# Performance work log

Measured on AMD Instinct MI355X. Metric: run time of the kernel, lower is better.

The kernel has to match this reference:

```python
import jax, jax.numpy as jnp
import numpy as np

SAMPLE_RATE = 16000
LOW_CUTOFF = 3400.0   # max(cutoff_freq) -> lowpass stage
HIGH_CUTOFF = 300.0   # min(cutoff_freq) -> highpass stage
Q = 0.7071067811865476  # torchaudio default Q = 1/sqrt(2)


def _lowpass_coeffs(cutoff, sr):
    w0 = 2.0 * np.pi * cutoff / sr
    alpha = np.sin(w0) / (2.0 * Q)
    cw = np.cos(w0)
    b0 = (1.0 - cw) / 2.0
    b1 = 1.0 - cw
    b2 = b0
    a0 = 1.0 + alpha
    a1 = -2.0 * cw
    a2 = 1.0 - alpha
    return tuple(np.float32(c / a0) for c in (b0, b1, b2, a1, a2))


def _highpass_coeffs(cutoff, sr):
    w0 = 2.0 * np.pi * cutoff / sr
    alpha = np.sin(w0) / (2.0 * Q)
    cw = np.cos(w0)
    b0 = (1.0 + cw) / 2.0
    b1 = -(1.0 + cw)
    b2 = b0
    a0 = 1.0 + alpha
    a1 = -2.0 * cw
    a2 = 1.0 - alpha
    return tuple(np.float32(c / a0) for c in (b0, b1, b2, a1, a2))


def _biquad(x, coeffs):
    """Direct-form-II-transposed biquad along the last (time) axis.
    x: [B, C, T]. Matches torchaudio lfilter with a0-normalized coeffs,
    followed by the torchaudio default clamp to [-1, 1]."""
    b0, b1, b2, a1, a2 = (jnp.asarray(c, x.dtype) for c in coeffs)
    xt = jnp.moveaxis(x, -1, 0)  # [T, B, C] for time scan

    def step(carry, xi):
        s1, s2 = carry
        y = b0 * xi + s1
        s1n = b1 * xi - a1 * y + s2
        s2n = b2 * xi - a2 * y
        return (s1n, s2n), y

    zeros = jnp.zeros(x.shape[:-1], x.dtype)
    _, yt = jax.lax.scan(step, (zeros, zeros), xt)
    y = jnp.moveaxis(yt, 0, -1)  # back to [B, C, T]
    return jnp.clip(y, -1.0, 1.0)


def setup_inputs() -> dict:
    key = jax.random.key(0)
    # scale down so the post-filter clamp to [-1,1] rarely saturates (audio-like amplitudes)
    waveform = 0.1 * jax.random.normal(key, (32, 2, 480000), dtype=jnp.float32)
    return {"waveform": waveform}


def reference(waveform):
    # bandpass = lowpass(max cutoff) then highpass(min cutoff)
    y = _biquad(waveform, _lowpass_coeffs(LOW_CUTOFF, SAMPLE_RATE))
    y = _biquad(y, _highpass_coeffs(HIGH_CUTOFF, SAMPLE_RATE))
    return y
```

## Files before the change

kernel.cpp:

```cpp
#include <hip/hip_runtime.h>
#include <math.h>


#define LCH   32
#define WUC   4
#define CPW   64
#define OUTC  (CPW - WUC)
#define SPAN  (OUTC * LCH)
#define T_LEN 480000
#define TILES (T_LEN / SPAN)
#define NTH   64

struct ScanConsts {
    float p[6][16];
    float e[LCH][4];
    float h[LCH];
    float kk[LCH][4];
};

#define PCOMB(P_, prev, val) {                                                                                \
        float4 nv;                                                                                            \
        nv.x = fmaf((P_)[ 0], prev.x, fmaf((P_)[ 1], prev.y, fmaf((P_)[ 2], prev.z, fmaf((P_)[ 3], prev.w, val.x)))); \
        nv.y = fmaf((P_)[ 4], prev.x, fmaf((P_)[ 5], prev.y, fmaf((P_)[ 6], prev.z, fmaf((P_)[ 7], prev.w, val.y)))); \
        nv.z = fmaf((P_)[ 8], prev.x, fmaf((P_)[ 9], prev.y, fmaf((P_)[10], prev.z, fmaf((P_)[11], prev.w, val.z)))); \
        nv.w = fmaf((P_)[12], prev.x, fmaf((P_)[13], prev.y, fmaf((P_)[14], prev.z, fmaf((P_)[15], prev.w, val.w)))); \
        val = nv;                                                                                             \
    }

__global__ __launch_bounds__(NTH, 4)
void bandpass_kernel(const float* __restrict__ in, float* __restrict__ out,
                     ScanConsts SC) {
    __shared__ float4 lds4[CPW * 9];
    const int lane    = threadIdx.x;
    const int wave_id = blockIdx.x;
    const int seq     = wave_id / TILES;
    const int tile    = wave_id - seq * TILES;
    const float* __restrict__ src = in  + (long)seq * T_LEN;
    float*       __restrict__ dst = out + (long)seq * T_LEN;

    const long tstart = (long)tile * SPAN - (long)(WUC * LCH);

    #pragma unroll
    for (int it = 0; it < 8; ++it) {
        int k = lane + it * NTH;
        long g = tstart + 4L * k;
        float4 v = make_float4(0.f, 0.f, 0.f, 0.f);
        if (g >= 0) v = *(const float4*)(src + g);
        lds4[9 * (k >> 3) + (k & 7)] = v;
    }
    __syncthreads();

    float xs[LCH];
    {
        const float4* cp = &lds4[9 * lane];
        #pragma unroll
        for (int q = 0; q < 8; ++q) {
            float4 v = cp[q];
            xs[4*q+0] = v.x; xs[4*q+1] = v.y; xs[4*q+2] = v.z; xs[4*q+3] = v.w;
        }
    }

    float4 val = make_float4(0.f, 0.f, 0.f, 0.f);
    #pragma unroll
    for (int j = 0; j < LCH; ++j) {
        const float* K = SC.kk[j];
        val.x = fmaf(K[0], xs[j], val.x);
        val.y = fmaf(K[1], xs[j], val.y);
        val.z = fmaf(K[2], xs[j], val.z);
        val.w = fmaf(K[3], xs[j], val.w);
    }

    #pragma unroll
    for (int k = 0; k < 6; ++k) {
        const int off = 1 << k;
        float4 prev;
        prev.x = __shfl_up(val.x, off);
        prev.y = __shfl_up(val.y, off);
        prev.z = __shfl_up(val.z, off);
        prev.w = __shfl_up(val.w, off);
        if (lane >= off) {
            const float* P_ = SC.p[k];
            PCOMB(P_, prev, val);
        }
    }
    float4 s0;
    s0.x = __shfl_up(val.x, 1);
    s0.y = __shfl_up(val.y, 1);
    s0.z = __shfl_up(val.z, 1);
    s0.w = __shfl_up(val.w, 1);
    if (lane == 0) s0 = make_float4(0.f, 0.f, 0.f, 0.f);

#define CONV1(i, dst_) {                                                              \
        const float* E = SC.e[i];                                                     \
        float acc = fmaf(E[0], s0.x, fmaf(E[1], s0.y, fmaf(E[2], s0.z, E[3]*s0.w)));  \
        _Pragma("unroll")                                                             \
        for (int j = 0; j <= (i); ++j) acc = fmaf(SC.h[(i)-j], xs[j], acc);           \
        dst_ = fminf(fmaxf(acc, -1.f), 1.f);                                          \
    }
    if (lane >= WUC) {
        float4* mp = &lds4[9 * lane];
        #pragma unroll
        for (int q = 0; q < 8; ++q) {
            float4 r;
            CONV1(4*q+0, r.x);
            CONV1(4*q+1, r.y);
            CONV1(4*q+2, r.z);
            CONV1(4*q+3, r.w);
            mp[q] = r;
        }
    }
#undef CONV1
    __syncthreads();

    const long ostart = (long)tile * SPAN;
    #pragma unroll
    for (int it = 0; it < 8; ++it) {
        int k = lane + it * NTH;
        if (k < SPAN / 4) {
            *(float4*)(dst + ostart + 4L * k) = lds4[9 * ((k >> 3) + WUC) + (k & 7)];
        }
    }
}
#undef PCOMB

static void biquad_coeffs_d(double cutoff, double sr, bool highpass, double* c) {
    const double Q  = 0.7071067811865476;
    const double w0 = 2.0 * M_PI * cutoff / sr;
    const double al = sin(w0) / (2.0 * Q);
    const double cw = cos(w0);
    double b0, b1, b2;
    if (highpass) { b0 = (1.0 + cw) / 2.0; b1 = -(1.0 + cw); b2 = b0; }
    else          { b0 = (1.0 - cw) / 2.0; b1 =  (1.0 - cw); b2 = b0; }
    const double a0 = 1.0 + al;
    c[0] = b0 / a0;
    c[1] = b1 / a0;
    c[2] = b2 / a0;
    c[3] = -(-2.0 * cw) / a0;
    c[4] = -(1.0 - al) / a0;
}

static void matmul4(const double* A, const double* B, double* C) {
    for (int r = 0; r < 4; ++r)
        for (int c = 0; c < 4; ++c) {
            double s = 0.0;
            for (int k = 0; k < 4; ++k) s += A[r * 4 + k] * B[k * 4 + c];
            C[r * 4 + c] = s;
        }
}

extern "C" void kernel_launch(void* const* d_in, const int* in_sizes, int n_in,
                              void* d_out, int out_size, void* d_ws, size_t ws_size,
                              hipStream_t stream) {
    const float* in  = (const float*)d_in[0];
    float*       out = (float*)d_out;

    double lpd[5], hpd[5];
    biquad_coeffs_d(3400.0, 16000.0, false, lpd);
    biquad_coeffs_d(300.0, 16000.0, true, hpd);

    ScanConsts SC;

    double M[16];
    for (int j = 0; j < 4; ++j) {
        double s1a = (j == 0), s2a = (j == 1), s1b = (j == 2), s2b = (j == 3);
        double y1  = s1a;
        double n1a = lpd[3] * y1 + s2a;
        double n2a = lpd[4] * y1;
        double y2  = hpd[0] * y1 + s1b;
        double n1b = hpd[1] * y1 + hpd[3] * y2 + s2b;
        double n2b = hpd[2] * y1 + hpd[4] * y2;
        M[0 * 4 + j] = n1a;
        M[1 * 4 + j] = n2a;
        M[2 * 4 + j] = n1b;
        M[3 * 4 + j] = n2b;
    }

    double A[16], T[16];
    for (int i = 0; i < 16; ++i) A[i] = M[i];
    for (int s = 0; s < 5; ++s) { matmul4(A, A, T); for (int i = 0; i < 16; ++i) A[i] = T[i]; }
    double Pk[16];
    for (int i = 0; i < 16; ++i) Pk[i] = A[i];
    for (int k = 0; k < 6; ++k) {
        for (int i = 0; i < 16; ++i) SC.p[k][i] = (float)Pk[i];
        matmul4(Pk, Pk, T);
        for (int i = 0; i < 16; ++i) Pk[i] = T[i];
    }

    for (int j = 0; j < 4; ++j) {
        double s1a = (j == 0), s2a = (j == 1), s1b = (j == 2), s2b = (j == 3);
        for (int i = 0; i < LCH; ++i) {
            double y1  = s1a;
            double n1a = lpd[3] * y1 + s2a;
            double n2a = lpd[4] * y1;
            double y2  = hpd[0] * y1 + s1b;
            double n1b = hpd[1] * y1 + hpd[3] * y2 + s2b;
            double n2b = hpd[2] * y1 + hpd[4] * y2;
            SC.e[i][j] = (float)y2;
            s1a = n1a; s2a = n2a; s1b = n1b; s2b = n2b;
        }
    }

    {
        double s1a = 0, s2a = 0, s1b = 0, s2b = 0;
        double Sarr[LCH][4];
        for (int n = 0; n < LCH; ++n) {
            double x   = (n == 0) ? 1.0 : 0.0;
            double y1  = lpd[0] * x + s1a;
            double n1a = lpd[1] * x + lpd[3] * y1 + s2a;
            double n2a = lpd[2] * x + lpd[4] * y1;
            double x2  = y1;
            double y2  = hpd[0] * x2 + s1b;
            double n1b = hpd[1] * x2 + hpd[3] * y2 + s2b;
            double n2b = hpd[2] * x2 + hpd[4] * y2;
            SC.h[n] = (float)y2;
            s1a = n1a; s2a = n2a; s1b = n1b; s2b = n2b;
            Sarr[n][0] = s1a; Sarr[n][1] = s2a; Sarr[n][2] = s1b; Sarr[n][3] = s2b;
        }
        for (int j = 0; j < LCH; ++j)
            for (int c = 0; c < 4; ++c)
                SC.kk[j][c] = (float)Sarr[LCH - 1 - j][c];
    }

    const int n_seq   = in_sizes[0] / T_LEN;
    const int n_blk   = n_seq * TILES;

    bandpass_kernel<<<dim3(n_blk), NTH, 0, stream>>>(in, out, SC);
}
```

Before: 225.4 us.

## Use persistent 4-wave blocks with register prefetch of the next tile

Moves from one 64-thread block per tile to a fixed grid of 1024 blocks of 256 threads, each wave looping over tiles in grid-stride order. The wave loads its next tile's input into registers while it computes the current tile, aiming to hide global-load latency and cut block launch overhead. Block-wide syncs are dropped because each wave uses its own LDS slice. This relies on intra-wave ordering of LDS accesses without a barrier, and the prefetch adds register pressure that could lower occupancy.

```diff
diff --git a/kernel.cpp b/kernel.cpp
--- a/kernel.cpp
+++ b/kernel.cpp
@@ -9,7 +9,9 @@
 #define SPAN  (OUTC * LCH)
 #define T_LEN 480000
 #define TILES (T_LEN / SPAN)
-#define NTH   64
+#define NTH   256
+#define WPB   4
+#define NBLK  1024
 
 struct ScanConsts {
     float p[6][16];
@@ -29,66 +31,94 @@
 
 __global__ __launch_bounds__(NTH, 4)
 void bandpass_kernel(const float* __restrict__ in, float* __restrict__ out,
-                     ScanConsts SC) {
-    __shared__ float4 lds4[CPW * 9];
-    const int lane    = threadIdx.x;
-    const int wave_id = blockIdx.x;
-    const int seq     = wave_id / TILES;
-    const int tile    = wave_id - seq * TILES;
-    const float* __restrict__ src = in  + (long)seq * T_LEN;
-    float*       __restrict__ dst = out + (long)seq * T_LEN;
-
-    const long tstart = (long)tile * SPAN - (long)(WUC * LCH);
-
-    #pragma unroll
-    for (int it = 0; it < 8; ++it) {
-        int k = lane + it * NTH;
-        long g = tstart + 4L * k;
-        float4 v = make_float4(0.f, 0.f, 0.f, 0.f);
-        if (g >= 0) v = *(const float4*)(src + g);
-        lds4[9 * (k >> 3) + (k & 7)] = v;
-    }
-    __syncthreads();
-
-    float xs[LCH];
-    {
-        const float4* cp = &lds4[9 * lane];
-        #pragma unroll
-        for (int q = 0; q < 8; ++q) {
-            float4 v = cp[q];
-            xs[4*q+0] = v.x; xs[4*q+1] = v.y; xs[4*q+2] = v.z; xs[4*q+3] = v.w;
-        }
-    }
-
-    float4 val = make_float4(0.f, 0.f, 0.f, 0.f);
-    #pragma unroll
-    for (int j = 0; j < LCH; ++j) {
-        const float* K = SC.kk[j];
-        val.x = fmaf(K[0], xs[j], val.x);
-        val.y = fmaf(K[1], xs[j], val.y);
-        val.z = fmaf(K[2], xs[j], val.z);
-        val.w = fmaf(K[3], xs[j], val.w);
-    }
-
-    #pragma unroll
-    for (int k = 0; k < 6; ++k) {
-        const int off = 1 << k;
-        float4 prev;
-        prev.x = __shfl_up(val.x, off);
-        prev.y = __shfl_up(val.y, off);
-        prev.z = __shfl_up(val.z, off);
-        prev.w = __shfl_up(val.w, off);
-        if (lane >= off) {
-            const float* P_ = SC.p[k];
-            PCOMB(P_, prev, val);
-        }
-    }
-    float4 s0;
-    s0.x = __shfl_up(val.x, 1);
-    s0.y = __shfl_up(val.y, 1);
-    s0.z = __shfl_up(val.z, 1);
-    s0.w = __shfl_up(val.w, 1);
-    if (lane == 0) s0 = make_float4(0.f, 0.f, 0.f, 0.f);
+                     ScanConsts SC, int n_tiles_total) {
+    __shared__ float4 ldsAll[WPB][CPW * 9];
+    const int lane  = threadIdx.x & 63;
+    const int wslot = threadIdx.x >> 6;
+    float4* __restrict__ lds4 = ldsAll[wslot];
+    const int NW = NBLK * WPB;
+    int tg = blockIdx.x * WPB + wslot;
+
+    float4 pre[8];
+    if (tg < n_tiles_total) {
+        const int seq  = tg / TILES;
+        const int tile = tg - seq * TILES;
+        const float* __restrict__ src = in + (long)seq * T_LEN;
+        const long tstart = (long)tile * SPAN - (long)(WUC * LCH);
+        #pragma unroll
+        for (int it = 0; it < 8; ++it) {
+            long g = tstart + 4L * (lane + 64 * it);
+            float4 v = make_float4(0.f, 0.f, 0.f, 0.f);
+            if (g >= 0) v = *(const float4*)(src + g);
+            pre[it] = v;
+        }
+    }
+
+    while (tg < n_tiles_total) {
+        const int seq  = tg / TILES;
+        const int tile = tg - seq * TILES;
+        float* __restrict__ dst = out + (long)seq * T_LEN;
+
+        #pragma unroll
+        for (int it = 0; it < 8; ++it) {
+            int k = lane + 64 * it;
+            lds4[9 * (k >> 3) + (k & 7)] = pre[it];
+        }
+
+        float xs[LCH];
+        {
+            const float4* cp = &lds4[9 * lane];
+            #pragma unroll
+            for (int q = 0; q < 8; ++q) {
+                float4 v = cp[q];
+                xs[4*q+0] = v.x; xs[4*q+1] = v.y; xs[4*q+2] = v.z; xs[4*q+3] = v.w;
+            }
+        }
+
+        const int tn = tg + NW;
+        if (tn < n_tiles_total) {
+            const int seq2  = tn / TILES;
+            const int tile2 = tn - seq2 * TILES;
+            const float* __restrict__ src2 = in + (long)seq2 * T_LEN;
+            const long ts2 = (long)tile2 * SPAN - (long)(WUC * LCH);
+            #pragma unroll
+            for (int it = 0; it < 8; ++it) {
+                long g = ts2 + 4L * (lane + 64 * it);
+                float4 v = make_float4(0.f, 0.f, 0.f, 0.f);
+                if (g >= 0) v = *(const float4*)(src2 + g);
+                pre[it] = v;
+            }
+        }
+
+        float4 val = make_float4(0.f, 0.f, 0.f, 0.f);
+        #pragma unroll
+        for (int j = 0; j < LCH; ++j) {
+            const float* K = SC.kk[j];
+            val.x = fmaf(K[0], xs[j], val.x);
+            val.y = fmaf(K[1], xs[j], val.y);
+            val.z = fmaf(K[2], xs[j], val.z);
+            val.w = fmaf(K[3], xs[j], val.w);
+        }
+
+        #pragma unroll
+        for (int k = 0; k < 6; ++k) {
+            const int off = 1 << k;
+            float4 prev;
+            prev.x = __shfl_up(val.x, off);
+            prev.y = __shfl_up(val.y, off);
+            prev.z = __shfl_up(val.z, off);
+            prev.w = __shfl_up(val.w, off);
+            if (lane >= off) {
+                const float* P_ = SC.p[k];
+                PCOMB(P_, prev, val);
+            }
+        }
+        float4 s0;
+        s0.x = __shfl_up(val.x, 1);
+        s0.y = __shfl_up(val.y, 1);
+        s0.z = __shfl_up(val.z, 1);
+        s0.w = __shfl_up(val.w, 1);
+        if (lane == 0) s0 = make_float4(0.f, 0.f, 0.f, 0.f);
 
 #define CONV1(i, dst_) {                                                              \
         const float* E = SC.e[i];                                                     \
@@ -97,28 +127,30 @@
         for (int j = 0; j <= (i); ++j) acc = fmaf(SC.h[(i)-j], xs[j], acc);           \
         dst_ = fminf(fmaxf(acc, -1.f), 1.f);                                          \
     }
-    if (lane >= WUC) {
-        float4* mp = &lds4[9 * lane];
-        #pragma unroll
-        for (int q = 0; q < 8; ++q) {
-            float4 r;
-            CONV1(4*q+0, r.x);
-            CONV1(4*q+1, r.y);
-            CONV1(4*q+2, r.z);
-            CONV1(4*q+3, r.w);
-            mp[q] = r;
-        }
-    }
+        if (lane >= WUC) {
+            float4* mp = &lds4[9 * lane];
+            #pragma unroll
+            for (int q = 0; q < 8; ++q) {
+                float4 r;
+                CONV1(4*q+0, r.x);
+                CONV1(4*q+1, r.y);
+                CONV1(4*q+2, r.z);
+                CONV1(4*q+3, r.w);
+                mp[q] = r;
+            }
+        }
 #undef CONV1
-    __syncthreads();
-
-    const long ostart = (long)tile * SPAN;
-    #pragma unroll
-    for (int it = 0; it < 8; ++it) {
-        int k = lane + it * NTH;
-        if (k < SPAN / 4) {
-            *(float4*)(dst + ostart + 4L * k) = lds4[9 * ((k >> 3) + WUC) + (k & 7)];
-        }
+
+        const long ostart = (long)tile * SPAN;
+        #pragma unroll
+        for (int it = 0; it < 8; ++it) {
+            int k = lane + 64 * it;
+            if (k < SPAN / 4) {
+                *(float4*)(dst + ostart + 4L * k) = lds4[9 * ((k >> 3) + WUC) + (k & 7)];
+            }
+        }
+
+        tg = tn;
     }
 }
 #undef PCOMB
@@ -221,8 +253,8 @@
                 SC.kk[j][c] = (float)Sarr[LCH - 1 - j][c];
     }
 
-    const int n_seq   = in_sizes[0] / T_LEN;
-    const int n_blk   = n_seq * TILES;
-
-    bandpass_kernel<<<dim3(n_blk), NTH, 0, stream>>>(in, out, SC);
-}
+    const int n_seq        = in_sizes[0] / T_LEN;
+    const int n_tiles_total = n_seq * TILES;
+
+    bandpass_kernel<<<dim3(NBLK), NTH, 0, stream>>>(in, out, SC, n_tiles_total);
+}
```

New measurement: 241.6 us. 7.2% more time.
